# Kernel optimization log

Hardware: AMD Instinct MI355X
Metric: run time of the kernel (lower is better)

Reference implementation:

```python
import jax, jax.numpy as jnp
import numpy as np

N = 100000
E = 1600000


def gcn_conv(x, W, b, src, dst, n_nodes):
    """PyG GCNConv: linear -> add self loops -> sym-normalized scatter-add."""
    h = x @ W  # [N, out]
    # degree with self-loops: deg[i] = 1 + in_degree(i)
    deg = jax.ops.segment_sum(jnp.ones((src.shape[0],), h.dtype), dst,
                              num_segments=n_nodes) + 1.0
    dinv = jax.lax.rsqrt(deg)  # deg >= 1 always
    norm = dinv[src] * dinv[dst]  # [E]
    # neighbor messages + self-loop contribution (norm = deg^-1)
    agg = jax.ops.segment_sum(h[src] * norm[:, None], dst,
                              num_segments=n_nodes)
    return agg + h * (dinv * dinv)[:, None] + b


def setup_inputs() -> dict:
    key = jax.random.key(0)
    k1, k2, k3, k4 = jax.random.split(key, 4)
    x = jax.random.normal(k1, (N, 128), dtype=jnp.float32)
    edge_index = jax.random.randint(k2, (2, E), 0, N, dtype=jnp.int64)
    W1 = jax.random.normal(k3, (128, 64), dtype=jnp.float32) * (1.0 / np.sqrt(128))
    b1 = jnp.zeros((64,), jnp.float32)
    W2 = jax.random.normal(k4, (64, 40), dtype=jnp.float32) * (1.0 / np.sqrt(64))
    b2 = jnp.zeros((40,), jnp.float32)
    return {"x": x, "edge_index": edge_index, "W1": W1, "b1": b1,
            "W2": W2, "b2": b2}


def reference(x, edge_index, W1, b1, W2, b2):
    src, dst = edge_index[0], edge_index[1]
    h = gcn_conv(x, W1, b1, src, dst, N)
    h = jax.nn.relu(h)
    # dropout is identity in eval mode; mask_features is a no-op
    h = gcn_conv(h, W2, b2, src, dst, N)
    return jax.nn.log_softmax(h, axis=1)
```

## Files before the change

kernel.cpp:

```cpp
#include <hip/hip_runtime.h>
#include <math.h>

#define N_NODES 100000
#define N_EDGES 1600000
#define F_IN    128
#define F_HID   64
#define F_OUT   40

#define BIN_SHIFT 9
#define NBINS     196
#define MAX_BIN   10240
#define FILL_BLOCKS 256

typedef unsigned int  uint;
typedef unsigned short ushort;
typedef __attribute__((ext_vector_type(8))) short bf16x8;
typedef __attribute__((ext_vector_type(4))) float f32x4;

__device__ __forceinline__ unsigned short f2bf(float f) {
    uint u = __float_as_uint(f);
    u = (u + 0x7FFF + ((u >> 16) & 1)) >> 16;
    return (unsigned short)u;
}
__device__ __forceinline__ uint pack2bf(float a, float b) {
    return (uint)f2bf(a) | ((uint)f2bf(b) << 16);
}
__device__ __forceinline__ float bf_lo(uint u) { return __uint_as_float(u << 16); }
__device__ __forceinline__ float bf_hi(uint u) { return __uint_as_float(u & 0xFFFF0000u); }

__global__ void bincount_kernel(const int* __restrict__ dst, int* __restrict__ bcount, int E) {
    __shared__ int lc[NBINS];
    int tid = threadIdx.x;
    for (int i = tid; i < NBINS; i += 256) lc[i] = 0;
    __syncthreads();
    int chunk = (E + gridDim.x - 1) / gridDim.x;
    int beg = blockIdx.x * chunk, end = min(E, beg + chunk);
    for (int e = beg + tid; e < end; e += 256)
        atomicAdd(&lc[dst[e] >> BIN_SHIFT], 1);
    __syncthreads();
    for (int i = tid; i < NBINS; i += 256)
        if (lc[i]) atomicAdd(&bcount[i], lc[i]);
}

__global__ void binscan_kernel(const int* __restrict__ bcount, int* __restrict__ bstart,
                               int* __restrict__ bcursor, int* __restrict__ rowstart) {
    __shared__ int tmp[256];
    int t = threadIdx.x;
    int v = (t < NBINS) ? bcount[t] : 0;
    tmp[t] = v;
    __syncthreads();
    for (int off = 1; off < 256; off <<= 1) {
        int u = (t >= off) ? tmp[t - off] : 0;
        __syncthreads();
        tmp[t] += u;
        __syncthreads();
    }
    if (t < NBINS) { int e = tmp[t] - v; bstart[t] = e; bcursor[t] = e; }
    if (t == 0) { bstart[NBINS] = N_EDGES; rowstart[N_NODES] = N_EDGES; }
}

__global__ void binfill_kernel(const int* __restrict__ src, const int* __restrict__ dst,
                               int* __restrict__ bcursor, int* __restrict__ bins, int E) {
    __shared__ int lcount[NBINS];
    __shared__ int gbase[NBINS];
    int tid = threadIdx.x;
    for (int i = tid; i < NBINS; i += 256) lcount[i] = 0;
    __syncthreads();
    int chunk = (E + gridDim.x - 1) / gridDim.x;
    int beg = blockIdx.x * chunk, end = min(E, beg + chunk);
    for (int e = beg + tid; e < end; e += 256)
        atomicAdd(&lcount[dst[e] >> BIN_SHIFT], 1);
    __syncthreads();
    for (int i = tid; i < NBINS; i += 256) {
        gbase[i] = lcount[i] ? atomicAdd(&bcursor[i], lcount[i]) : 0;
        lcount[i] = 0;
    }
    __syncthreads();
    for (int e = beg + tid; e < end; e += 256) {
        int d = dst[e];
        int b = d >> BIN_SHIFT;
        int p = atomicAdd(&lcount[b], 1);
        bins[gbase[b] + p] = src[e] | ((d & 511) << 17);
    }
}

__global__ void binsort_kernel(const int* __restrict__ bstart, const int* __restrict__ bins,
                               int* __restrict__ csr, int* __restrict__ rowstart,
                               float* __restrict__ dinv) {
    __shared__ int hist[512];
    __shared__ int scan[512];
    __shared__ int cur[512];
    __shared__ int sorted[MAX_BIN];
    int b = blockIdx.x, t = threadIdx.x;
    int base = bstart[b], cnt = bstart[b + 1] - base;
    hist[t] = 0;
    __syncthreads();
    for (int i = t; i < cnt; i += 512)
        atomicAdd(&hist[(unsigned)bins[base + i] >> 17], 1);
    __syncthreads();
    int v = hist[t];
    scan[t] = v;
    __syncthreads();
    for (int off = 1; off < 512; off <<= 1) {
        int u = (t >= off) ? scan[t - off] : 0;
        __syncthreads();
        scan[t] += u;
        __syncthreads();
    }
    int excl = scan[t] - v;
    cur[t] = excl;
    int node = (b << BIN_SHIFT) + t;
    if (node < N_NODES) {
        rowstart[node] = base + excl;
        dinv[node] = rsqrtf((float)v + 1.0f);
    }
    __syncthreads();
    for (int i = t; i < cnt; i += 512) {
        int p   = bins[base + i];
        int pos = atomicAdd(&cur[(unsigned)p >> 17], 1);
        sorted[pos] = p & 0x1FFFF;
    }
    __syncthreads();
    for (int i = t; i < cnt; i += 512)
        csr[base + i] = sorted[i];
}

__global__ void wtrans_kernel(const float* __restrict__ W, uint* __restrict__ Wt) {
    int tid = threadIdx.x;
    for (int i = tid; i < 4096; i += 256) {
        int c  = i >> 6;
        int kp = i & 63;
        Wt[i] = pack2bf(W[(2 * kp) * F_HID + c], W[(2 * kp + 1) * F_HID + c]);
    }
}

#define XPITCH 68
__global__ __launch_bounds__(256) void gemm1_kernel(const float* __restrict__ x,
                                                    const uint* __restrict__ Wt,
                                                    ushort* __restrict__ h, int n) {
    __shared__ __align__(16) uint Xu[64 * XPITCH];
    __shared__ __align__(16) uint Wu[64 * XPITCH];
    int tid = threadIdx.x;
    int node0 = blockIdx.x * 64;

    {
        int c = tid >> 2, qq = tid & 3;
        const uint4* gsrc = (const uint4*)&Wt[c * 64 + qq * 16];
        uint4* ldst = (uint4*)&Wu[c * XPITCH + qq * 16];
        #pragma unroll
        for (int j = 0; j < 4; ++j) ldst[j] = gsrc[j];
    }
    {
        int row = tid >> 2, qq = tid & 3;
        int node = node0 + row;
        uint4* ldst = (uint4*)&Xu[row * XPITCH + qq * 16];
        if (node < n) {
            const float4* gsrc = (const float4*)&x[(size_t)node * F_IN + qq * 32];
            #pragma unroll
            for (int j = 0; j < 4; ++j) {
                float4 a = gsrc[2 * j], b = gsrc[2 * j + 1];
                uint4 o;
                o.x = pack2bf(a.x, a.y); o.y = pack2bf(a.z, a.w);
                o.z = pack2bf(b.x, b.y); o.w = pack2bf(b.z, b.w);
                ldst[j] = o;
            }
        } else {
            uint4 z = make_uint4(0, 0, 0, 0);
            #pragma unroll
            for (int j = 0; j < 4; ++j) ldst[j] = z;
        }
    }
    __syncthreads();

    int wv   = tid >> 6;
    int lane = tid & 63;
    int lrow = lane & 15;
    int quad = lane >> 4;

    bf16x8 bfrag[4][4];
    #pragma unroll
    for (int t = 0; t < 4; ++t)
        #pragma unroll
        for (int s = 0; s < 4; ++s)
            bfrag[t][s] = *(const bf16x8*)&Wu[(t * 16 + lrow) * XPITCH + s * 16 + quad * 4];

    f32x4 acc[4];
    #pragma unroll
    for (int t = 0; t < 4; ++t) acc[t] = (f32x4){0.f, 0.f, 0.f, 0.f};

    #pragma unroll
    for (int s = 0; s < 4; ++s) {
        bf16x8 afrag = *(const bf16x8*)&Xu[(wv * 16 + lrow) * XPITCH + s * 16 + quad * 4];
        #pragma unroll
        for (int t = 0; t < 4; ++t)
            acc[t] = __builtin_amdgcn_mfma_f32_16x16x32_bf16(afrag, bfrag[t][s], acc[t], 0, 0, 0);
    }

    #pragma unroll
    for (int t = 0; t < 4; ++t) {
        #pragma unroll
        for (int i = 0; i < 4; ++i) {
            int node = node0 + wv * 16 + quad * 4 + i;
            if (node < n) h[(size_t)node * F_HID + t * 16 + lrow] = f2bf(acc[t][i]);
        }
    }
}

__global__ void agg1_kernel(const int* __restrict__ rowstart, const int* __restrict__ csr,
                            const float* __restrict__ dinv, const ushort* __restrict__ h,
                            const float* __restrict__ b, ushort* __restrict__ out, int n) {
    int node = blockIdx.x * 4 + (threadIdx.x >> 6);
    int lane = threadIdx.x & 63;
    if (node >= n) return;
    int slot = lane >> 3;
    int c    = lane & 7;
    int beg = rowstart[node], end = rowstart[node + 1];
    float acc[8] = {0.f,0.f,0.f,0.f,0.f,0.f,0.f,0.f};
    for (int base = beg; base < end; base += 64) {
        int idx = base + lane;
        int   sid = 0; float wgt = 0.f;
        if (idx < end) { sid = csr[idx]; wgt = dinv[sid]; }
        int cnt    = min(64, end - base);
        int groups = (cnt + 7) >> 3;
        int g = 0;
        for (; g + 2 <= groups; g += 2) {
            int   sA = __shfl(sid, g * 8 + slot);
            float wA = __shfl(wgt, g * 8 + slot);
            int   sB = __shfl(sid, g * 8 + 8 + slot);
            float wB = __shfl(wgt, g * 8 + 8 + slot);
            uint4 hA = *(const uint4*)&h[(size_t)sA * F_HID + (c << 3)];
            uint4 hB = *(const uint4*)&h[(size_t)sB * F_HID + (c << 3)];
            acc[0] += bf_lo(hA.x) * wA; acc[1] += bf_hi(hA.x) * wA;
            acc[2] += bf_lo(hA.y) * wA; acc[3] += bf_hi(hA.y) * wA;
            acc[4] += bf_lo(hA.z) * wA; acc[5] += bf_hi(hA.z) * wA;
            acc[6] += bf_lo(hA.w) * wA; acc[7] += bf_hi(hA.w) * wA;
            acc[0] += bf_lo(hB.x) * wB; acc[1] += bf_hi(hB.x) * wB;
            acc[2] += bf_lo(hB.y) * wB; acc[3] += bf_hi(hB.y) * wB;
            acc[4] += bf_lo(hB.z) * wB; acc[5] += bf_hi(hB.z) * wB;
            acc[6] += bf_lo(hB.w) * wB; acc[7] += bf_hi(hB.w) * wB;
        }
        if (g < groups) {
            int   sA = __shfl(sid, g * 8 + slot);
            float wA = __shfl(wgt, g * 8 + slot);
            uint4 hA = *(const uint4*)&h[(size_t)sA * F_HID + (c << 3)];
            acc[0] += bf_lo(hA.x) * wA; acc[1] += bf_hi(hA.x) * wA;
            acc[2] += bf_lo(hA.y) * wA; acc[3] += bf_hi(hA.y) * wA;
            acc[4] += bf_lo(hA.z) * wA; acc[5] += bf_hi(hA.z) * wA;
            acc[6] += bf_lo(hA.w) * wA; acc[7] += bf_hi(hA.w) * wA;
        }
    }
    #pragma unroll
    for (int m = 8; m < 64; m <<= 1) {
        #pragma unroll
        for (int k = 0; k < 8; ++k) acc[k] += __shfl_xor(acc[k], m);
    }
    if (slot == 0) {
        float di = dinv[node];
        uint4 hs = *(const uint4*)&h[(size_t)node * F_HID + (c << 3)];
        float self[8] = { bf_lo(hs.x), bf_hi(hs.x), bf_lo(hs.y), bf_hi(hs.y),
                          bf_lo(hs.z), bf_hi(hs.z), bf_lo(hs.w), bf_hi(hs.w) };
        float4 b0 = *(const float4*)&b[c << 3];
        float4 b1v = *(const float4*)&b[(c << 3) + 4];
        float bb[8] = { b0.x, b0.y, b0.z, b0.w, b1v.x, b1v.y, b1v.z, b1v.w };
        ushort o[8];
        #pragma unroll
        for (int k = 0; k < 8; ++k) {
            float v = fmaxf(acc[k] * di + self[k] * di * di + bb[k], 0.f);
            o[k] = f2bf(v);
        }
        uint4 pk;
        pk.x = (uint)o[0] | ((uint)o[1] << 16);
        pk.y = (uint)o[2] | ((uint)o[3] << 16);
        pk.z = (uint)o[4] | ((uint)o[5] << 16);
        pk.w = (uint)o[6] | ((uint)o[7] << 16);
        *(uint4*)&out[(size_t)node * F_HID + (c << 3)] = pk;
    }
}

__global__ void gemm2_kernel(const ushort* __restrict__ a, const float* __restrict__ W,
                             ushort* __restrict__ h, int n) {
    __shared__ float Wl[F_HID * F_OUT];
    int tid = threadIdx.x;
    for (int i = tid; i < F_HID * F_OUT; i += 256) Wl[i] = W[i];
    __syncthreads();
    long long idx = (long long)blockIdx.x * 256 + tid;
    if (idx >= (long long)n * F_OUT) return;
    int node = (int)(idx / F_OUT);
    int col  = (int)(idx - (long long)node * F_OUT);
    const uint* arow = (const uint*)(a + (size_t)node * F_HID);
    float acc = 0.0f;
    #pragma unroll 8
    for (int k = 0; k < F_HID / 2; ++k) {
        uint u = arow[k];
        acc += bf_lo(u) * Wl[(2 * k) * F_OUT + col] + bf_hi(u) * Wl[(2 * k + 1) * F_OUT + col];
    }
    h[idx] = f2bf(acc);
}

__global__ void agg2_kernel(const int* __restrict__ rowstart, const int* __restrict__ csr,
                            const float* __restrict__ dinv, const ushort* __restrict__ h,
                            const float* __restrict__ b, float* __restrict__ out, int n) {
    int node = blockIdx.x * 4 + (threadIdx.x >> 6);
    int lane = threadIdx.x & 63;
    if (node >= n) return;
    int slot = lane / 10;
    int c    = lane - slot * 10;
    int beg = rowstart[node], end = rowstart[node + 1];
    float acc[4] = {0.f, 0.f, 0.f, 0.f};
    for (int base = beg; base < end; base += 60) {
        int idx = base + lane;
        int   sid = 0; float wgt = 0.f;
        if (lane < 60 && idx < end) { sid = csr[idx]; wgt = dinv[sid]; }
        int cnt    = min(60, end - base);
        int groups = (cnt + 5) / 6;
        int slbase = (slot < 6) ? slot : 60;
        int g = 0;
        for (; g + 2 <= groups; g += 2) {
            int   slA = (slot < 6) ? (g * 6 + slot) : 60;
            int   slB = (slot < 6) ? (g * 6 + 6 + slot) : 60;
            int   sA = __shfl(sid, slA);
            float wA = __shfl(wgt, slA);
            int   sB = __shfl(sid, slB);
            float wB = __shfl(wgt, slB);
            uint2 hA = *(const uint2*)&h[(size_t)sA * F_OUT + (c << 2)];
            uint2 hB = *(const uint2*)&h[(size_t)sB * F_OUT + (c << 2)];
            acc[0] += bf_lo(hA.x) * wA; acc[1] += bf_hi(hA.x) * wA;
            acc[2] += bf_lo(hA.y) * wA; acc[3] += bf_hi(hA.y) * wA;
            acc[0] += bf_lo(hB.x) * wB; acc[1] += bf_hi(hB.x) * wB;
            acc[2] += bf_lo(hB.y) * wB; acc[3] += bf_hi(hB.y) * wB;
        }
        if (g < groups) {
            int   slA = (slot < 6) ? (g * 6 + slot) : 60;
            int   sA = __shfl(sid, slA);
            float wA = __shfl(wgt, slA);
            uint2 hA = *(const uint2*)&h[(size_t)sA * F_OUT + (c << 2)];
            acc[0] += bf_lo(hA.x) * wA; acc[1] += bf_hi(hA.x) * wA;
            acc[2] += bf_lo(hA.y) * wA; acc[3] += bf_hi(hA.y) * wA;
        }
        (void)slbase;
    }
    float r[4];
    #pragma unroll
    for (int k = 0; k < 4; ++k) {
        float t3 = __shfl(acc[k], lane + 30);
        float s0 = acc[k] + t3;
        float t1 = __shfl(s0, lane + 10);
        float t2 = __shfl(s0, lane + 20);
        r[k] = s0 + t1 + t2;
    }
    float val[4] = {0.f, 0.f, 0.f, 0.f};
    float m = -INFINITY;
    if (lane < 10) {
        float di = dinv[node];
        uint2 hs = *(const uint2*)&h[(size_t)node * F_OUT + (c << 2)];
        float self[4] = { bf_lo(hs.x), bf_hi(hs.x), bf_lo(hs.y), bf_hi(hs.y) };
        float4 bb = *(const float4*)&b[c << 2];
        float bbv[4] = { bb.x, bb.y, bb.z, bb.w };
        #pragma unroll
        for (int k = 0; k < 4; ++k) {
            val[k] = r[k] * di + self[k] * di * di + bbv[k];
            m = fmaxf(m, val[k]);
        }
    }
    #pragma unroll
    for (int off = 1; off < 16; off <<= 1) m = fmaxf(m, __shfl_xor(m, off));
    float p = 0.f;
    if (lane < 10)
        p = __expf(val[0] - m) + __expf(val[1] - m) + __expf(val[2] - m) + __expf(val[3] - m);
    #pragma unroll
    for (int off = 1; off < 16; off <<= 1) p += __shfl_xor(p, off);
    float lse = m + __logf(p);
    if (lane < 10) {
        float4 o;
        o.x = val[0] - lse; o.y = val[1] - lse; o.z = val[2] - lse; o.w = val[3] - lse;
        *(float4*)&out[(size_t)node * F_OUT + (c << 2)] = o;
    }
}

extern "C" void kernel_launch(void* const* d_in, const int* in_sizes, int n_in,
                              void* d_out, int out_size, void* d_ws, size_t ws_size,
                              hipStream_t stream) {
    const float* x  = (const float*)d_in[0];
    const int*   ei = (const int*)d_in[1];
    const float* W1 = (const float*)d_in[2];
    const float* b1 = (const float*)d_in[3];
    const float* W2 = (const float*)d_in[4];
    const float* b2 = (const float*)d_in[5];
    const int* src = ei;
    const int* dst = ei + N_EDGES;

    char* p = (char*)d_ws;
    int*    bcount   = (int*)p;     p += (size_t)(NBINS + 4) * 4;
    int*    bstart   = (int*)p;     p += (size_t)(NBINS + 4) * 4;
    int*    bcursor  = (int*)p;     p += (size_t)(NBINS + 4) * 4;
    int*    bins     = (int*)p;     p += (size_t)N_EDGES * 4;
    int*    csr_src  = (int*)p;     p += (size_t)N_EDGES * 4;
    int*    rowstart = (int*)p;     p += (size_t)(N_NODES + 4) * 4;
    float*  dinv     = (float*)p;   p += (size_t)N_NODES * 4;
    uint*   Wtb      = (uint*)p;    p += (size_t)4096 * 4;
    ushort* h1b      = (ushort*)p;  p += (size_t)N_NODES * F_HID * 2;
    ushort* out1b    = (ushort*)p;  p += (size_t)N_NODES * F_HID * 2;
    ushort* h2b      = (ushort*)p;  p += (size_t)N_NODES * F_OUT * 2;
    float*  out      = (float*)d_out;

    hipMemsetAsync(bcount, 0, (size_t)NBINS * 4, stream);

    bincount_kernel<<<FILL_BLOCKS, 256, 0, stream>>>(dst, bcount, N_EDGES);
    binscan_kernel <<<1, 256, 0, stream>>>(bcount, bstart, bcursor, rowstart);
    binfill_kernel <<<FILL_BLOCKS, 256, 0, stream>>>(src, dst, bcursor, bins, N_EDGES);
    binsort_kernel <<<NBINS, 512, 0, stream>>>(bstart, bins, csr_src, rowstart, dinv);
    wtrans_kernel<<<1, 256, 0, stream>>>(W1, Wtb);
    gemm1_kernel<<<(N_NODES + 63) / 64, 256, 0, stream>>>(x, Wtb, h1b, N_NODES);
    agg1_kernel <<<(N_NODES + 3) / 4, 256, 0, stream>>>(rowstart, csr_src, dinv, h1b, b1,
                                                        out1b, N_NODES);
    gemm2_kernel<<<((N_NODES * F_OUT) + 255) / 256, 256, 0, stream>>>(out1b, W2, h2b, N_NODES);
    agg2_kernel <<<(N_NODES + 3) / 4, 256, 0, stream>>>(rowstart, csr_src, dinv, h2b, b2,
                                                        out, N_NODES);
}
```

Baseline: 296.8 us.

## Use fixed-capacity edge bins and widen per-node aggregation work

Replaces the count, scan and memset passes with fixed-capacity bins at b*BIN_CAP, so the fill kernel advances cursors from preset offsets and the sort uses the final cursor as the bin count. A per-node row count array replaces rowstart[node+1] because rows are no longer contiguous across bins. Both aggregation kernels now process four nodes per wave, and agg2 uses 8-wide bf16 loads with 12 edges in flight per group. This removes two launches and one pass over the dst array. The cost is that correctness depends on no bin exceeding BIN_CAP edges, which holds for uniform random inputs but is not guaranteed in general.

```diff
diff --git a/kernel.cpp b/kernel.cpp
--- a/kernel.cpp
+++ b/kernel.cpp
@@ -9,7 +9,7 @@
 
 #define BIN_SHIFT 9
 #define NBINS     196
-#define MAX_BIN   10240
+#define BIN_CAP   10240
 #define FILL_BLOCKS 256
 
 typedef unsigned int  uint;
@@ -28,35 +28,9 @@
 __device__ __forceinline__ float bf_lo(uint u) { return __uint_as_float(u << 16); }
 __device__ __forceinline__ float bf_hi(uint u) { return __uint_as_float(u & 0xFFFF0000u); }
 
-__global__ void bincount_kernel(const int* __restrict__ dst, int* __restrict__ bcount, int E) {
-    __shared__ int lc[NBINS];
-    int tid = threadIdx.x;
-    for (int i = tid; i < NBINS; i += 256) lc[i] = 0;
-    __syncthreads();
-    int chunk = (E + gridDim.x - 1) / gridDim.x;
-    int beg = blockIdx.x * chunk, end = min(E, beg + chunk);
-    for (int e = beg + tid; e < end; e += 256)
-        atomicAdd(&lc[dst[e] >> BIN_SHIFT], 1);
-    __syncthreads();
-    for (int i = tid; i < NBINS; i += 256)
-        if (lc[i]) atomicAdd(&bcount[i], lc[i]);
-}
-
-__global__ void binscan_kernel(const int* __restrict__ bcount, int* __restrict__ bstart,
-                               int* __restrict__ bcursor, int* __restrict__ rowstart) {
-    __shared__ int tmp[256];
+__global__ void init_kernel(int* __restrict__ bcursor) {
     int t = threadIdx.x;
-    int v = (t < NBINS) ? bcount[t] : 0;
-    tmp[t] = v;
-    __syncthreads();
-    for (int off = 1; off < 256; off <<= 1) {
-        int u = (t >= off) ? tmp[t - off] : 0;
-        __syncthreads();
-        tmp[t] += u;
-        __syncthreads();
-    }
-    if (t < NBINS) { int e = tmp[t] - v; bstart[t] = e; bcursor[t] = e; }
-    if (t == 0) { bstart[NBINS] = N_EDGES; rowstart[N_NODES] = N_EDGES; }
+    if (t < NBINS) bcursor[t] = t * BIN_CAP;
 }
 
 __global__ void binfill_kernel(const int* __restrict__ src, const int* __restrict__ dst,
@@ -84,15 +58,16 @@
     }
 }
 
-__global__ void binsort_kernel(const int* __restrict__ bstart, const int* __restrict__ bins,
+__global__ void binsort_kernel(const int* __restrict__ bcursor, const int* __restrict__ bins,
                                int* __restrict__ csr, int* __restrict__ rowstart,
-                               float* __restrict__ dinv) {
+                               int* __restrict__ rowcnt, float* __restrict__ dinv) {
     __shared__ int hist[512];
     __shared__ int scan[512];
     __shared__ int cur[512];
-    __shared__ int sorted[MAX_BIN];
+    __shared__ int sorted[BIN_CAP];
     int b = blockIdx.x, t = threadIdx.x;
-    int base = bstart[b], cnt = bstart[b + 1] - base;
+    int base = b * BIN_CAP;
+    int cnt = bcursor[b] - base;
     hist[t] = 0;
     __syncthreads();
     for (int i = t; i < cnt; i += 512)
@@ -112,6 +87,7 @@
     int node = (b << BIN_SHIFT) + t;
     if (node < N_NODES) {
         rowstart[node] = base + excl;
+        rowcnt[node]   = v;
         dinv[node] = rsqrtf((float)v + 1.0f);
     }
     __syncthreads();
@@ -206,74 +182,79 @@
     }
 }
 
-__global__ void agg1_kernel(const int* __restrict__ rowstart, const int* __restrict__ csr,
-                            const float* __restrict__ dinv, const ushort* __restrict__ h,
-                            const float* __restrict__ b, ushort* __restrict__ out, int n) {
-    int node = blockIdx.x * 4 + (threadIdx.x >> 6);
+__global__ void agg1_kernel(const int* __restrict__ rowstart, const int* __restrict__ rowcnt,
+                            const int* __restrict__ csr, const float* __restrict__ dinv,
+                            const ushort* __restrict__ h, const float* __restrict__ b,
+                            ushort* __restrict__ out, int n) {
+    int wv   = threadIdx.x >> 6;
     int lane = threadIdx.x & 63;
-    if (node >= n) return;
     int slot = lane >> 3;
     int c    = lane & 7;
-    int beg = rowstart[node], end = rowstart[node + 1];
-    float acc[8] = {0.f,0.f,0.f,0.f,0.f,0.f,0.f,0.f};
-    for (int base = beg; base < end; base += 64) {
-        int idx = base + lane;
-        int   sid = 0; float wgt = 0.f;
-        if (idx < end) { sid = csr[idx]; wgt = dinv[sid]; }
-        int cnt    = min(64, end - base);
-        int groups = (cnt + 7) >> 3;
-        int g = 0;
-        for (; g + 2 <= groups; g += 2) {
-            int   sA = __shfl(sid, g * 8 + slot);
-            float wA = __shfl(wgt, g * 8 + slot);
-            int   sB = __shfl(sid, g * 8 + 8 + slot);
-            float wB = __shfl(wgt, g * 8 + 8 + slot);
-            uint4 hA = *(const uint4*)&h[(size_t)sA * F_HID + (c << 3)];
-            uint4 hB = *(const uint4*)&h[(size_t)sB * F_HID + (c << 3)];
-            acc[0] += bf_lo(hA.x) * wA; acc[1] += bf_hi(hA.x) * wA;
-            acc[2] += bf_lo(hA.y) * wA; acc[3] += bf_hi(hA.y) * wA;
-            acc[4] += bf_lo(hA.z) * wA; acc[5] += bf_hi(hA.z) * wA;
-            acc[6] += bf_lo(hA.w) * wA; acc[7] += bf_hi(hA.w) * wA;
-            acc[0] += bf_lo(hB.x) * wB; acc[1] += bf_hi(hB.x) * wB;
-            acc[2] += bf_lo(hB.y) * wB; acc[3] += bf_hi(hB.y) * wB;
-            acc[4] += bf_lo(hB.z) * wB; acc[5] += bf_hi(hB.z) * wB;
-            acc[6] += bf_lo(hB.w) * wB; acc[7] += bf_hi(hB.w) * wB;
-        }
-        if (g < groups) {
-            int   sA = __shfl(sid, g * 8 + slot);
-            float wA = __shfl(wgt, g * 8 + slot);
-            uint4 hA = *(const uint4*)&h[(size_t)sA * F_HID + (c << 3)];
-            acc[0] += bf_lo(hA.x) * wA; acc[1] += bf_hi(hA.x) * wA;
-            acc[2] += bf_lo(hA.y) * wA; acc[3] += bf_hi(hA.y) * wA;
-            acc[4] += bf_lo(hA.z) * wA; acc[5] += bf_hi(hA.z) * wA;
-            acc[6] += bf_lo(hA.w) * wA; acc[7] += bf_hi(hA.w) * wA;
-        }
-    }
-    #pragma unroll
-    for (int m = 8; m < 64; m <<= 1) {
-        #pragma unroll
-        for (int k = 0; k < 8; ++k) acc[k] += __shfl_xor(acc[k], m);
-    }
-    if (slot == 0) {
-        float di = dinv[node];
-        uint4 hs = *(const uint4*)&h[(size_t)node * F_HID + (c << 3)];
-        float self[8] = { bf_lo(hs.x), bf_hi(hs.x), bf_lo(hs.y), bf_hi(hs.y),
-                          bf_lo(hs.z), bf_hi(hs.z), bf_lo(hs.w), bf_hi(hs.w) };
-        float4 b0 = *(const float4*)&b[c << 3];
-        float4 b1v = *(const float4*)&b[(c << 3) + 4];
-        float bb[8] = { b0.x, b0.y, b0.z, b0.w, b1v.x, b1v.y, b1v.z, b1v.w };
-        ushort o[8];
-        #pragma unroll
-        for (int k = 0; k < 8; ++k) {
-            float v = fmaxf(acc[k] * di + self[k] * di * di + bb[k], 0.f);
-            o[k] = f2bf(v);
-        }
-        uint4 pk;
-        pk.x = (uint)o[0] | ((uint)o[1] << 16);
-        pk.y = (uint)o[2] | ((uint)o[3] << 16);
-        pk.z = (uint)o[4] | ((uint)o[5] << 16);
-        pk.w = (uint)o[6] | ((uint)o[7] << 16);
-        *(uint4*)&out[(size_t)node * F_HID + (c << 3)] = pk;
+    int node0 = blockIdx.x * 16 + wv * 4;
+    for (int nn = 0; nn < 4; ++nn) {
+        int node = node0 + nn;
+        if (node >= n) break;
+        int beg = rowstart[node], end = beg + rowcnt[node];
+        float acc[8] = {0.f,0.f,0.f,0.f,0.f,0.f,0.f,0.f};
+        for (int base = beg; base < end; base += 64) {
+            int idx = base + lane;
+            int   sid = 0; float wgt = 0.f;
+            if (idx < end) { sid = csr[idx]; wgt = dinv[sid]; }
+            int cnt    = min(64, end - base);
+            int groups = (cnt + 7) >> 3;
+            int g = 0;
+            for (; g + 2 <= groups; g += 2) {
+                int   sA = __shfl(sid, g * 8 + slot);
+                float wA = __shfl(wgt, g * 8 + slot);
+                int   sB = __shfl(sid, g * 8 + 8 + slot);
+                float wB = __shfl(wgt, g * 8 + 8 + slot);
+                uint4 hA = *(const uint4*)&h[(size_t)sA * F_HID + (c << 3)];
+                uint4 hB = *(const uint4*)&h[(size_t)sB * F_HID + (c << 3)];
+                acc[0] += bf_lo(hA.x) * wA; acc[1] += bf_hi(hA.x) * wA;
+                acc[2] += bf_lo(hA.y) * wA; acc[3] += bf_hi(hA.y) * wA;
+                acc[4] += bf_lo(hA.z) * wA; acc[5] += bf_hi(hA.z) * wA;
+                acc[6] += bf_lo(hA.w) * wA; acc[7] += bf_hi(hA.w) * wA;
+                acc[0] += bf_lo(hB.x) * wB; acc[1] += bf_hi(hB.x) * wB;
+                acc[2] += bf_lo(hB.y) * wB; acc[3] += bf_hi(hB.y) * wB;
+                acc[4] += bf_lo(hB.z) * wB; acc[5] += bf_hi(hB.z) * wB;
+                acc[6] += bf_lo(hB.w) * wB; acc[7] += bf_hi(hB.w) * wB;
+            }
+            if (g < groups) {
+                int   sA = __shfl(sid, g * 8 + slot);
+                float wA = __shfl(wgt, g * 8 + slot);
+                uint4 hA = *(const uint4*)&h[(size_t)sA * F_HID + (c << 3)];
+                acc[0] += bf_lo(hA.x) * wA; acc[1] += bf_hi(hA.x) * wA;
+                acc[2] += bf_lo(hA.y) * wA; acc[3] += bf_hi(hA.y) * wA;
+                acc[4] += bf_lo(hA.z) * wA; acc[5] += bf_hi(hA.z) * wA;
+                acc[6] += bf_lo(hA.w) * wA; acc[7] += bf_hi(hA.w) * wA;
+            }
+        }
+        #pragma unroll
+        for (int m = 8; m < 64; m <<= 1) {
+            #pragma unroll
+            for (int k = 0; k < 8; ++k) acc[k] += __shfl_xor(acc[k], m);
+        }
+        if (slot == 0) {
+            float di = dinv[node];
+            uint4 hs = *(const uint4*)&h[(size_t)node * F_HID + (c << 3)];
+            float self[8] = { bf_lo(hs.x), bf_hi(hs.x), bf_lo(hs.y), bf_hi(hs.y),
+                              bf_lo(hs.z), bf_hi(hs.z), bf_lo(hs.w), bf_hi(hs.w) };
+            float4 b0 = *(const float4*)&b[c << 3];
+            float4 b1v = *(const float4*)&b[(c << 3) + 4];
+            float bb[8] = { b0.x, b0.y, b0.z, b0.w, b1v.x, b1v.y, b1v.z, b1v.w };
+            ushort o[8];
+            #pragma unroll
+            for (int k = 0; k < 8; ++k) {
+                float v = fmaxf(acc[k] * di + self[k] * di * di + bb[k], 0.f);
+                o[k] = f2bf(v);
+            }
+            uint4 pk;
+            pk.x = (uint)o[0] | ((uint)o[1] << 16);
+            pk.y = (uint)o[2] | ((uint)o[3] << 16);
+            pk.z = (uint)o[4] | ((uint)o[5] << 16);
+            pk.w = (uint)o[6] | ((uint)o[7] << 16);
+            *(uint4*)&out[(size_t)node * F_HID + (c << 3)] = pk;
+        }
     }
 }
 
@@ -297,83 +278,104 @@
     h[idx] = f2bf(acc);
 }
 
-__global__ void agg2_kernel(const int* __restrict__ rowstart, const int* __restrict__ csr,
-                            const float* __restrict__ dinv, const ushort* __restrict__ h,
-                            const float* __restrict__ b, float* __restrict__ out, int n) {
-    int node = blockIdx.x * 4 + (threadIdx.x >> 6);
+__global__ void agg2_kernel(const int* __restrict__ rowstart, const int* __restrict__ rowcnt,
+                            const int* __restrict__ csr, const float* __restrict__ dinv,
+                            const ushort* __restrict__ h, const float* __restrict__ b,
+                            float* __restrict__ out, int n) {
+    int wv   = threadIdx.x >> 6;
     int lane = threadIdx.x & 63;
-    if (node >= n) return;
-    int slot = lane / 10;
-    int c    = lane - slot * 10;
-    int beg = rowstart[node], end = rowstart[node + 1];
-    float acc[4] = {0.f, 0.f, 0.f, 0.f};
-    for (int base = beg; base < end; base += 60) {
-        int idx = base + lane;
-        int   sid = 0; float wgt = 0.f;
-        if (lane < 60 && idx < end) { sid = csr[idx]; wgt = dinv[sid]; }
-        int cnt    = min(60, end - base);
-        int groups = (cnt + 5) / 6;
-        int slbase = (slot < 6) ? slot : 60;
-        int g = 0;
-        for (; g + 2 <= groups; g += 2) {
-            int   slA = (slot < 6) ? (g * 6 + slot) : 60;
-            int   slB = (slot < 6) ? (g * 6 + 6 + slot) : 60;
-            int   sA = __shfl(sid, slA);
-            float wA = __shfl(wgt, slA);
-            int   sB = __shfl(sid, slB);
-            float wB = __shfl(wgt, slB);
-            uint2 hA = *(const uint2*)&h[(size_t)sA * F_OUT + (c << 2)];
-            uint2 hB = *(const uint2*)&h[(size_t)sB * F_OUT + (c << 2)];
-            acc[0] += bf_lo(hA.x) * wA; acc[1] += bf_hi(hA.x) * wA;
-            acc[2] += bf_lo(hA.y) * wA; acc[3] += bf_hi(hA.y) * wA;
-            acc[0] += bf_lo(hB.x) * wB; acc[1] += bf_hi(hB.x) * wB;
-            acc[2] += bf_lo(hB.y) * wB; acc[3] += bf_hi(hB.y) * wB;
-        }
-        if (g < groups) {
-            int   slA = (slot < 6) ? (g * 6 + slot) : 60;
-            int   sA = __shfl(sid, slA);
-            float wA = __shfl(wgt, slA);
-            uint2 hA = *(const uint2*)&h[(size_t)sA * F_OUT + (c << 2)];
-            acc[0] += bf_lo(hA.x) * wA; acc[1] += bf_hi(hA.x) * wA;
-            acc[2] += bf_lo(hA.y) * wA; acc[3] += bf_hi(hA.y) * wA;
-        }
-        (void)slbase;
-    }
-    float r[4];
-    #pragma unroll
-    for (int k = 0; k < 4; ++k) {
-        float t3 = __shfl(acc[k], lane + 30);
-        float s0 = acc[k] + t3;
-        float t1 = __shfl(s0, lane + 10);
-        float t2 = __shfl(s0, lane + 20);
-        r[k] = s0 + t1 + t2;
-    }
-    float val[4] = {0.f, 0.f, 0.f, 0.f};
-    float m = -INFINITY;
-    if (lane < 10) {
-        float di = dinv[node];
-        uint2 hs = *(const uint2*)&h[(size_t)node * F_OUT + (c << 2)];
-        float self[4] = { bf_lo(hs.x), bf_hi(hs.x), bf_lo(hs.y), bf_hi(hs.y) };
-        float4 bb = *(const float4*)&b[c << 2];
-        float bbv[4] = { bb.x, bb.y, bb.z, bb.w };
-        #pragma unroll
-        for (int k = 0; k < 4; ++k) {
-            val[k] = r[k] * di + self[k] * di * di + bbv[k];
-            m = fmaxf(m, val[k]);
-        }
-    }
-    #pragma unroll
-    for (int off = 1; off < 16; off <<= 1) m = fmaxf(m, __shfl_xor(m, off));
-    float p = 0.f;
-    if (lane < 10)
-        p = __expf(val[0] - m) + __expf(val[1] - m) + __expf(val[2] - m) + __expf(val[3] - m);
-    #pragma unroll
-    for (int off = 1; off < 16; off <<= 1) p += __shfl_xor(p, off);
-    float lse = m + __logf(p);
-    if (lane < 10) {
-        float4 o;
-        o.x = val[0] - lse; o.y = val[1] - lse; o.z = val[2] - lse; o.w = val[3] - lse;
-        *(float4*)&out[(size_t)node * F_OUT + (c << 2)] = o;
+    int slot = lane / 5;
+    int c    = lane - slot * 5;
+    int node0 = blockIdx.x * 16 + wv * 4;
+    float bb[8];
+    if (lane < 5) {
+        float4 b0 = *(const float4*)&b[lane * 8];
+        float4 b1 = *(const float4*)&b[lane * 8 + 4];
+        bb[0] = b0.x; bb[1] = b0.y; bb[2] = b0.z; bb[3] = b0.w;
+        bb[4] = b1.x; bb[5] = b1.y; bb[6] = b1.z; bb[7] = b1.w;
+    }
+    for (int nn = 0; nn < 4; ++nn) {
+        int node = node0 + nn;
+        if (node >= n) break;
+        int beg = rowstart[node], end = beg + rowcnt[node];
+        float acc[8] = {0.f,0.f,0.f,0.f,0.f,0.f,0.f,0.f};
+        for (int base = beg; base < end; base += 60) {
+            int idx = base + lane;
+            int   sid = 0; float wgt = 0.f;
+            if (lane < 60 && idx < end) { sid = csr[idx]; wgt = dinv[sid]; }
+            int cnt    = min(60, end - base);
+            int groups = (cnt + 11) / 12;
+            int g = 0;
+            for (; g + 2 <= groups; g += 2) {
+                int   slA = (slot < 12) ? (g * 12 + slot) : 60;
+                int   slB = (slot < 12) ? (g * 12 + 12 + slot) : 60;
+                int   sA = __shfl(sid, slA);
+                float wA = __shfl(wgt, slA);
+                int   sB = __shfl(sid, slB);
+                float wB = __shfl(wgt, slB);
+                uint4 hA = *(const uint4*)&h[(size_t)sA * F_OUT + c * 8];
+                uint4 hB = *(const uint4*)&h[(size_t)sB * F_OUT + c * 8];
+                acc[0] += bf_lo(hA.x) * wA; acc[1] += bf_hi(hA.x) * wA;
+                acc[2] += bf_lo(hA.y) * wA; acc[3] += bf_hi(hA.y) * wA;
+                acc[4] += bf_lo(hA.z) * wA; acc[5] += bf_hi(hA.z) * wA;
+                acc[6] += bf_lo(hA.w) * wA; acc[7] += bf_hi(hA.w) * wA;
+                acc[0] += bf_lo(hB.x) * wB; acc[1] += bf_hi(hB.x) * wB;
+                acc[2] += bf_lo(hB.y) * wB; acc[3] += bf_hi(hB.y) * wB;
+                acc[4] += bf_lo(hB.z) * wB; acc[5] += bf_hi(hB.z) * wB;
+                acc[6] += bf_lo(hB.w) * wB; acc[7] += bf_hi(hB.w) * wB;
+            }
+            if (g < groups) {
+                int   slA = (slot < 12) ? (g * 12 + slot) : 60;
+                int   sA = __shfl(sid, slA);
+                float wA = __shfl(wgt, slA);
+                uint4 hA = *(const uint4*)&h[(size_t)sA * F_OUT + c * 8];
+                acc[0] += bf_lo(hA.x) * wA; acc[1] += bf_hi(hA.x) * wA;
+                acc[2] += bf_lo(hA.y) * wA; acc[3] += bf_hi(hA.y) * wA;
+                acc[4] += bf_lo(hA.z) * wA; acc[5] += bf_hi(hA.z) * wA;
+                acc[6] += bf_lo(hA.w) * wA; acc[7] += bf_hi(hA.w) * wA;
+            }
+        }
+        float r[8];
+        #pragma unroll
+        for (int k = 0; k < 8; ++k) {
+            float t6 = __shfl(acc[k], lane + 30);
+            float s6 = acc[k] + t6;
+            float t3 = __shfl(s6, lane + 15);
+            float s3 = s6 + t3;
+            float t1 = __shfl(s3, lane + 5);
+            float t2 = __shfl(s3, lane + 10);
+            r[k] = s3 + t1 + t2;
+        }
+        float val[8];
+        float m = -INFINITY;
+        if (lane < 5) {
+            float di = dinv[node];
+            uint4 hs = *(const uint4*)&h[(size_t)node * F_OUT + lane * 8];
+            float self[8] = { bf_lo(hs.x), bf_hi(hs.x), bf_lo(hs.y), bf_hi(hs.y),
+                              bf_lo(hs.z), bf_hi(hs.z), bf_lo(hs.w), bf_hi(hs.w) };
+            #pragma unroll
+            for (int k = 0; k < 8; ++k) {
+                val[k] = r[k] * di + self[k] * di * di + bb[k];
+                m = fmaxf(m, val[k]);
+            }
+        }
+        #pragma unroll
+        for (int off = 1; off < 8; off <<= 1) m = fmaxf(m, __shfl_xor(m, off));
+        float p = 0.f;
+        if (lane < 5) {
+            #pragma unroll
+            for (int k = 0; k < 8; ++k) p += __expf(val[k] - m);
+        }
+        #pragma unroll
+        for (int off = 1; off < 8; off <<= 1) p += __shfl_xor(p, off);
+        float lse = m + __logf(p);
+        if (lane < 5) {
+            float4 o0, o1;
+            o0.x = val[0] - lse; o0.y = val[1] - lse; o0.z = val[2] - lse; o0.w = val[3] - lse;
+            o1.x = val[4] - lse; o1.y = val[5] - lse; o1.z = val[6] - lse; o1.w = val[7] - lse;
+            *(float4*)&out[(size_t)node * F_OUT + lane * 8]     = o0;
+            *(float4*)&out[(size_t)node * F_OUT + lane * 8 + 4] = o1;
+        }
     }
 }
 
@@ -390,12 +392,11 @@
     const int* dst = ei + N_EDGES;
 
     char* p = (char*)d_ws;
-    int*    bcount   = (int*)p;     p += (size_t)(NBINS + 4) * 4;
-    int*    bstart   = (int*)p;     p += (size_t)(NBINS + 4) * 4;
     int*    bcursor  = (int*)p;     p += (size_t)(NBINS + 4) * 4;
-    int*    bins     = (int*)p;     p += (size_t)N_EDGES * 4;
-    int*    csr_src  = (int*)p;     p += (size_t)N_EDGES * 4;
+    int*    bins     = (int*)p;     p += (size_t)NBINS * BIN_CAP * 4;
+    int*    csr_src  = (int*)p;     p += (size_t)NBINS * BIN_CAP * 4;
     int*    rowstart = (int*)p;     p += (size_t)(N_NODES + 4) * 4;
+    int*    rowcnt   = (int*)p;     p += (size_t)(N_NODES + 4) * 4;
     float*  dinv     = (float*)p;   p += (size_t)N_NODES * 4;
     uint*   Wtb      = (uint*)p;    p += (size_t)4096 * 4;
     ushort* h1b      = (ushort*)p;  p += (size_t)N_NODES * F_HID * 2;
@@ -403,17 +404,14 @@
     ushort* h2b      = (ushort*)p;  p += (size_t)N_NODES * F_OUT * 2;
     float*  out      = (float*)d_out;
 
-    hipMemsetAsync(bcount, 0, (size_t)NBINS * 4, stream);
-
-    bincount_kernel<<<FILL_BLOCKS, 256, 0, stream>>>(dst, bcount, N_EDGES);
-    binscan_kernel <<<1, 256, 0, stream>>>(bcount, bstart, bcursor, rowstart);
-    binfill_kernel <<<FILL_BLOCKS, 256, 0, stream>>>(src, dst, bcursor, bins, N_EDGES);
-    binsort_kernel <<<NBINS, 512, 0, stream>>>(bstart, bins, csr_src, rowstart, dinv);
-    wtrans_kernel<<<1, 256, 0, stream>>>(W1, Wtb);
-    gemm1_kernel<<<(N_NODES + 63) / 64, 256, 0, stream>>>(x, Wtb, h1b, N_NODES);
-    agg1_kernel <<<(N_NODES + 3) / 4, 256, 0, stream>>>(rowstart, csr_src, dinv, h1b, b1,
-                                                        out1b, N_NODES);
-    gemm2_kernel<<<((N_NODES * F_OUT) + 255) / 256, 256, 0, stream>>>(out1b, W2, h2b, N_NODES);
-    agg2_kernel <<<(N_NODES + 3) / 4, 256, 0, stream>>>(rowstart, csr_src, dinv, h2b, b2,
-                                                        out, N_NODES);
-}
+    init_kernel   <<<1, 256, 0, stream>>>(bcursor);
+    binfill_kernel<<<FILL_BLOCKS, 256, 0, stream>>>(src, dst, bcursor, bins, N_EDGES);
+    binsort_kernel<<<NBINS, 512, 0, stream>>>(bcursor, bins, csr_src, rowstart, rowcnt, dinv);
+    wtrans_kernel <<<1, 256, 0, stream>>>(W1, Wtb);
+    gemm1_kernel  <<<(N_NODES + 63) / 64, 256, 0, stream>>>(x, Wtb, h1b, N_NODES);
+    agg1_kernel   <<<(N_NODES + 15) / 16, 256, 0, stream>>>(rowstart, rowcnt, csr_src, dinv,
+                                                            h1b, b1, out1b, N_NODES);
+    gemm2_kernel  <<<((N_NODES * F_OUT) + 255) / 256, 256, 0, stream>>>(out1b, W2, h2b, N_NODES);
+    agg2_kernel   <<<(N_NODES + 15) / 16, 256, 0, stream>>>(rowstart, rowcnt, csr_src, dinv,
+                                                            h2b, b2, out, N_NODES);
+}
```

Measured after the change: 303.0 us. +2.1%, slower.
